# Kernel tuning notes

Measured on AMD Instinct MI355X. Metric: run time of the kernel, lower is better.

## Reference

```python
import jax, jax.numpy as jnp
import numpy as np

EPS = 1e-5


def _gcn_conv(h, W, b, src, dst, norm, N):
    # h: (B, N, F_in) -> linear transform then normalized neighbor aggregation
    h = h @ W                                  # (B, N, H)
    msg = h[:, src, :] * norm[None, :, None]   # gather + edge norm, (B, E, H)
    agg = jax.vmap(lambda m: jax.ops.segment_sum(m, dst, num_segments=N))(msg)
    return agg + b


def _batchnorm(h, gamma, beta):
    # BatchNorm1d over flattened (B*N, H), training-mode batch statistics
    B, N, H = h.shape
    f = h.reshape(-1, H)
    mean = f.mean(axis=0)
    var = f.var(axis=0)
    f = (f - mean) * jax.lax.rsqrt(var + EPS) * gamma + beta
    return f.reshape(B, N, H)


def setup_inputs() -> dict:
    key = jax.random.key(0)
    ks = jax.random.split(key, 6)
    B, N, E, IN, H, OUT = 2, 20000, 640000, 128, 128, 10
    x = jax.random.normal(ks[0], (B, N, IN), dtype=jnp.float32)
    edge_index = jax.random.randint(ks[1], (2, E), 0, N, dtype=jnp.int64)
    W1 = jax.random.normal(ks[2], (IN, H), dtype=jnp.float32) / np.sqrt(IN)
    W2 = jax.random.normal(ks[3], (H, H), dtype=jnp.float32) / np.sqrt(H)
    Wc = jax.random.normal(ks[4], (H, OUT), dtype=jnp.float32) / np.sqrt(H)
    return {
        "x": x,
        "W1": W1, "b1": jnp.zeros((H,), jnp.float32),
        "W2": W2, "b2": jnp.zeros((H,), jnp.float32),
        "g1": jnp.ones((H,), jnp.float32), "bt1": jnp.zeros((H,), jnp.float32),
        "g2": jnp.ones((H,), jnp.float32), "bt2": jnp.zeros((H,), jnp.float32),
        "Wc": Wc, "bc": jnp.zeros((OUT,), jnp.float32),
        "edge_index": edge_index,
    }


def reference(x, W1, b1, W2, b2, g1, bt1, g2, bt2, Wc, bc, edge_index):
    N = x.shape[1]
    loops = jnp.arange(N, dtype=edge_index.dtype)
    src = jnp.concatenate([edge_index[0], loops])  # add self-loops (GCNConv default)
    dst = jnp.concatenate([edge_index[1], loops])
    deg = jax.ops.segment_sum(jnp.ones(src.shape[0], x.dtype), dst, num_segments=N)
    dinv = jnp.where(deg > 0, jax.lax.rsqrt(deg), 0.0)
    norm = dinv[src] * dinv[dst]                   # symmetric GCN normalization

    h = jax.nn.relu(_gcn_conv(x, W1, b1, src, dst, norm, N))
    h = _batchnorm(h, g1, bt1)
    # dropout is identity in eval mode
    h = jax.nn.relu(_gcn_conv(h, W2, b2, src, dst, norm, N))
    h = _batchnorm(h, g2, bt2)
    return h @ Wc + bc                              # (B, N, out_dim)
```

## Files before the change

kernel.cpp:

```cpp
#include <hip/hip_runtime.h>
#include <hip/hip_bf16.h>


constexpr int Nn   = 20000;
constexpr int Ee   = 640000;
constexpr int OUTd = 10;
constexpr int Mm   = 2 * Nn;
constexpr int ELLW = 96;
constexpr int NSLOT = 64;
constexpr int NP   = 8;
constexpr int PSZ  = Nn / NP;
constexpr int NSEG = (Ee + 2047) / 2048;
constexpr int SCB  = NSEG * NP;
constexpr int GMB  = Mm / 64;
#define EPSV 1e-5f
constexpr float INV_M = 1.0f / (float)Mm;

using frag16 = __attribute__((ext_vector_type(8))) short;
using f32x4  = __attribute__((ext_vector_type(4))) float;

__device__ inline short bf(float f) {
    union { __hip_bfloat16 h; short s; } u;
    u.h = __float2bfloat16(f);
    return u.s;
}
__device__ inline float lo16(unsigned u) { union { unsigned v; float f; } x; x.v = u << 16;        return x.f; }
__device__ inline float hi16(unsigned u) { union { unsigned v; float f; } x; x.v = u & 0xffff0000u; return x.f; }
__device__ inline unsigned pack2(float f0, float f1) {
    return (unsigned)(unsigned short)bf(f0) | ((unsigned)(unsigned short)bf(f1) << 16);
}
__device__ inline float wdeg(int c) { return rsqrtf((float)c + 1.0f); }

__global__ __launch_bounds__(256) void fg1_k(const int* __restrict__ src, const int* __restrict__ dst,
                                             int* __restrict__ cnt, int* __restrict__ ell,
                                             const float* __restrict__ A,
                                             const float* __restrict__ W,
                                             unsigned short* __restrict__ Hout) {
    __shared__ short Wl[128 * 136];
    int t = threadIdx.x;

    if (blockIdx.x >= GMB) {
        int s   = blockIdx.x - GMB;
        int p   = blockIdx.x & 7;
        int seg = s >> 3;
        int lo  = p * PSZ, hi = lo + PSZ;
        int base = seg * 2048 + t;
        #pragma unroll
        for (int it = 0; it < 8; ++it) {
            int e = base + it * 256;
            if (e < Ee) {
                int d = dst[e];
                if (d >= lo && d < hi) {
                    int pos = atomicAdd(&cnt[d], 1);
                    if (pos < ELLW) ell[(size_t)d * ELLW + pos] = src[e];
                }
            }
        }
        return;
    }

    int bid = blockIdx.x;

    for (int it = 0; it < 8; ++it) {
        int lin = it * 256 + t;
        int kp  = lin & 63;
        int n4  = (lin >> 6) * 4;
        float4 w0 = *(const float4*)(W + (size_t)(2 * kp) * 128 + n4);
        float4 w1 = *(const float4*)(W + (size_t)(2 * kp + 1) * 128 + n4);
        *(unsigned*)&Wl[(n4 + 0) * 136 + 2 * kp] = pack2(w0.x, w1.x);
        *(unsigned*)&Wl[(n4 + 1) * 136 + 2 * kp] = pack2(w0.y, w1.y);
        *(unsigned*)&Wl[(n4 + 2) * 136 + 2 * kp] = pack2(w0.z, w1.z);
        *(unsigned*)&Wl[(n4 + 3) * 136 + 2 * kp] = pack2(w0.w, w1.w);
    }
    __syncthreads();

    int wv = t >> 6, l = t & 63;
    int row_q = l >> 4, lane16 = l & 15;
    int row0 = bid * 64 + wv * 16;

    frag16 a[4];
    const float* Arow = A + (size_t)(row0 + lane16) * 128;
    #pragma unroll
    for (int q = 0; q < 4; ++q) {
        int k0 = q * 32 + row_q * 8;
        float4 v0 = *(const float4*)(Arow + k0);
        float4 v1 = *(const float4*)(Arow + k0 + 4);
        frag16 fa = { bf(v0.x), bf(v0.y), bf(v0.z), bf(v0.w),
                      bf(v1.x), bf(v1.y), bf(v1.z), bf(v1.w) };
        a[q] = fa;
    }

    f32x4 acc[8];
    #pragma unroll
    for (int c = 0; c < 8; ++c) acc[c] = (f32x4){0.f, 0.f, 0.f, 0.f};

    #pragma unroll
    for (int c = 0; c < 8; ++c) {
        int n = c * 16 + lane16;
        #pragma unroll
        for (int q = 0; q < 4; ++q) {
            int k0 = q * 32 + row_q * 8;
            frag16 b = *(const frag16*)&Wl[n * 136 + k0];
            acc[c] = __builtin_amdgcn_mfma_f32_16x16x32_bf16(a[q], b, acc[c], 0, 0, 0);
        }
    }

    #pragma unroll
    for (int r = 0; r < 4; ++r) {
        int rg = row0 + row_q * 4 + r;
        int b  = rg >= Nn;
        int n  = rg - b * Nn;
        unsigned short* dstp = Hout + (size_t)n * 256 + b * 128;
        #pragma unroll
        for (int c = 0; c < 8; ++c)
            dstp[c * 16 + lane16] = (unsigned short)bf(acc[c][r]);
    }
}

__global__ __launch_bounds__(256) void gemm2_k(const unsigned short* __restrict__ Abf,
                                               const float* __restrict__ W,
                                               const float* __restrict__ g,
                                               const float* __restrict__ bt,
                                               const float* __restrict__ S,
                                               const int* __restrict__ cnt,
                                               unsigned short* __restrict__ Hout) {
    __shared__ short Wl[128 * 136];
    __shared__ float al[128], cl[128], dpart[2][128];
    int t = threadIdx.x;

    if (t < 128) {
        float s = 0.f, ss = 0.f;
        #pragma unroll 8
        for (int k = 0; k < NSLOT; ++k) {
            s  += S[k * 256 + t];
            ss += S[k * 256 + 128 + t];
        }
        float m   = s * INV_M;
        float var = ss * INV_M - m * m;
        float a   = g[t] * rsqrtf(var + EPSV);
        float c   = bt[t] - m * a;
        al[t] = a; cl[t] = c;
    }
    __syncthreads();

    for (int it = 0; it < 8; ++it) {
        int lin = it * 256 + t;
        int kp  = lin & 63;
        int n4  = (lin >> 6) * 4;
        float a0 = al[2 * kp], a1 = al[2 * kp + 1];
        float4 w0 = *(const float4*)(W + (size_t)(2 * kp) * 128 + n4);
        float4 w1 = *(const float4*)(W + (size_t)(2 * kp + 1) * 128 + n4);
        w0.x *= a0; w0.y *= a0; w0.z *= a0; w0.w *= a0;
        w1.x *= a1; w1.y *= a1; w1.z *= a1; w1.w *= a1;
        *(unsigned*)&Wl[(n4 + 0) * 136 + 2 * kp] = pack2(w0.x, w1.x);
        *(unsigned*)&Wl[(n4 + 1) * 136 + 2 * kp] = pack2(w0.y, w1.y);
        *(unsigned*)&Wl[(n4 + 2) * 136 + 2 * kp] = pack2(w0.z, w1.z);
        *(unsigned*)&Wl[(n4 + 3) * 136 + 2 * kp] = pack2(w0.w, w1.w);
    }

    {
        int col = t & 127, hh = t >> 7;
        const float* Wc0 = W + (size_t)(hh * 64) * 128 + col;
        float dp = 0.f;
        #pragma unroll 8
        for (int k = 0; k < 64; ++k) dp += cl[hh * 64 + k] * Wc0[(size_t)k * 128];
        dpart[hh][col] = dp;
    }
    __syncthreads();

    int wv = t >> 6, l = t & 63;
    int row_q = l >> 4, lane16 = l & 15;
    int row0 = blockIdx.x * 64 + wv * 16;

    int rgA = row0 + lane16;
    int bA  = rgA >= Nn;
    int nA  = rgA - bA * Nn;
    const unsigned short* Arow = Abf + (size_t)nA * 256 + bA * 128;
    frag16 a[4];
    #pragma unroll
    for (int q = 0; q < 4; ++q) {
        int k0 = q * 32 + row_q * 8;
        a[q] = *(const frag16*)(Arow + k0);
    }

    f32x4 acc[8];
    #pragma unroll
    for (int c = 0; c < 8; ++c) {
        int n = c * 16 + lane16;
        float d = dpart[0][n] + dpart[1][n];
        acc[c] = (f32x4){d, d, d, d};
    }

    #pragma unroll
    for (int c = 0; c < 8; ++c) {
        int n = c * 16 + lane16;
        #pragma unroll
        for (int q = 0; q < 4; ++q) {
            int k0 = q * 32 + row_q * 8;
            frag16 b = *(const frag16*)&Wl[n * 136 + k0];
            acc[c] = __builtin_amdgcn_mfma_f32_16x16x32_bf16(a[q], b, acc[c], 0, 0, 0);
        }
    }

    #pragma unroll
    for (int r = 0; r < 4; ++r) {
        int rg = row0 + row_q * 4 + r;
        int b  = rg >= Nn;
        int n  = rg - b * Nn;
        float dv = wdeg(cnt[n]);
        unsigned short* dst = Hout + (size_t)n * 256 + b * 128;
        #pragma unroll
        for (int c = 0; c < 8; ++c)
            dst[c * 16 + lane16] = (unsigned short)bf(acc[c][r] * dv);
    }
}

__device__ inline void accw(const uint4& v, float w,
                            float& a0, float& a1, float& a2, float& a3,
                            float& a4, float& a5, float& a6, float& a7) {
    a0 = fmaf(w, lo16(v.x), a0); a1 = fmaf(w, hi16(v.x), a1);
    a2 = fmaf(w, lo16(v.y), a2); a3 = fmaf(w, hi16(v.y), a3);
    a4 = fmaf(w, lo16(v.z), a4); a5 = fmaf(w, hi16(v.z), a5);
    a6 = fmaf(w, lo16(v.w), a6); a7 = fmaf(w, hi16(v.w), a7);
}
__device__ inline void acc8(const uint4& v,
                            float& a0, float& a1, float& a2, float& a3,
                            float& a4, float& a5, float& a6, float& a7) {
    a0 += lo16(v.x); a1 += hi16(v.x);
    a2 += lo16(v.y); a3 += hi16(v.y);
    a4 += lo16(v.z); a5 += hi16(v.z);
    a6 += lo16(v.w); a7 += hi16(v.w);
}

__device__ inline void stats_epilogue(int t, int wv, int l, int g, unsigned bslot,
                                      float o0, float o1, float o2, float o3,
                                      float o4, float o5, float o6, float o7,
                                      float* __restrict__ S) {
    float q0 = o0 * o0, q1 = o1 * o1, q2 = o2 * o2, q3 = o3 * o3;
    float q4 = o4 * o4, q5 = o5 * o5, q6 = o6 * o6, q7 = o7 * o7;
    float s0 = o0 + __shfl_xor(o0, 16), s1 = o1 + __shfl_xor(o1, 16);
    float s2 = o2 + __shfl_xor(o2, 16), s3 = o3 + __shfl_xor(o3, 16);
    float s4 = o4 + __shfl_xor(o4, 16), s5 = o5 + __shfl_xor(o5, 16);
    float s6 = o6 + __shfl_xor(o6, 16), s7 = o7 + __shfl_xor(o7, 16);
    float t0 = q0 + __shfl_xor(q0, 16), t1 = q1 + __shfl_xor(q1, 16);
    float t2 = q2 + __shfl_xor(q2, 16), t3 = q3 + __shfl_xor(q3, 16);
    float t4 = q4 + __shfl_xor(q4, 16), t5 = q5 + __shfl_xor(q5, 16);
    float t6 = q6 + __shfl_xor(q6, 16), t7 = q7 + __shfl_xor(q7, 16);

    __shared__ float sh[4][16][17];
    if (l < 16) {
        float* p = sh[wv][l];
        p[0] = s0; p[1] = s1; p[2] = s2; p[3] = s3;
        p[4] = s4; p[5] = s5; p[6] = s6; p[7] = s7;
        p[8]  = t0; p[9]  = t1; p[10] = t2; p[11] = t3;
        p[12] = t4; p[13] = t5; p[14] = t6; p[15] = t7;
    }
    __syncthreads();
    int col  = t & 127, stat = t >> 7;
    int gi   = col >> 3, slot = (col & 7) + stat * 8;
    float v = sh[0][gi][slot] + sh[1][gi][slot] + sh[2][gi][slot] + sh[3][gi][slot];
    atomicAdd(&S[bslot * 256 + stat * 128 + col], v);
}

__global__ __launch_bounds__(256) void agg1_k(const unsigned short* __restrict__ h,
                                              const int* __restrict__ ell,
                                              const int* __restrict__ cnt,
                                              const float* __restrict__ bias,
                                              unsigned short* __restrict__ act,
                                              float* __restrict__ S) {
    int t  = threadIdx.x;
    int wv = t >> 6;
    int l  = t & 63;
    int n  = __builtin_amdgcn_readfirstlane(blockIdx.x * 4 + wv);
    int half = l >> 5;
    int g    = l & 31;

    const uint4* h4 = (const uint4*)h;

    float a0 = 0.f, a1 = 0.f, a2 = 0.f, a3 = 0.f, a4 = 0.f, a5 = 0.f, a6 = 0.f, a7 = 0.f;

    int degc = cnt[n];
    float dn = wdeg(degc);
    int deg = degc > ELLW ? ELLW : degc;
    const int* row = ell + (size_t)n * ELLW;

    uint4 u = h4[(size_t)n * 32 + g];

    int j = 0;
    for (; j + 15 < deg; j += 16) {
        int i0 = row[j +  0 + half], i1 = row[j +  2 + half];
        int i2 = row[j +  4 + half], i3 = row[j +  6 + half];
        int i4 = row[j +  8 + half], i5 = row[j + 10 + half];
        int i6 = row[j + 12 + half], i7 = row[j + 14 + half];
        int c0 = cnt[i0], c1 = cnt[i1], c2 = cnt[i2], c3 = cnt[i3];
        int c4 = cnt[i4], c5 = cnt[i5], c6 = cnt[i6], c7 = cnt[i7];
        uint4 v0 = h4[(size_t)i0 * 32 + g];
        uint4 v1 = h4[(size_t)i1 * 32 + g];
        uint4 v2 = h4[(size_t)i2 * 32 + g];
        uint4 v3 = h4[(size_t)i3 * 32 + g];
        uint4 v4 = h4[(size_t)i4 * 32 + g];
        uint4 v5 = h4[(size_t)i5 * 32 + g];
        uint4 v6 = h4[(size_t)i6 * 32 + g];
        uint4 v7 = h4[(size_t)i7 * 32 + g];
        accw(v0, wdeg(c0), a0, a1, a2, a3, a4, a5, a6, a7);
        accw(v1, wdeg(c1), a0, a1, a2, a3, a4, a5, a6, a7);
        accw(v2, wdeg(c2), a0, a1, a2, a3, a4, a5, a6, a7);
        accw(v3, wdeg(c3), a0, a1, a2, a3, a4, a5, a6, a7);
        accw(v4, wdeg(c4), a0, a1, a2, a3, a4, a5, a6, a7);
        accw(v5, wdeg(c5), a0, a1, a2, a3, a4, a5, a6, a7);
        accw(v6, wdeg(c6), a0, a1, a2, a3, a4, a5, a6, a7);
        accw(v7, wdeg(c7), a0, a1, a2, a3, a4, a5, a6, a7);
    }
    for (; j + 3 < deg; j += 4) {
        int i0 = row[j + half];
        int i1 = row[j + 2 + half];
        int c0 = cnt[i0], c1 = cnt[i1];
        uint4 v0 = h4[(size_t)i0 * 32 + g];
        uint4 v1 = h4[(size_t)i1 * 32 + g];
        accw(v0, wdeg(c0), a0, a1, a2, a3, a4, a5, a6, a7);
        accw(v1, wdeg(c1), a0, a1, a2, a3, a4, a5, a6, a7);
    }
    for (; j + 1 < deg; j += 2) {
        int i0 = row[j + half];
        int c0 = cnt[i0];
        uint4 v0 = h4[(size_t)i0 * 32 + g];
        accw(v0, wdeg(c0), a0, a1, a2, a3, a4, a5, a6, a7);
    }
    if (j < deg && half == 0) {
        int i0 = row[j];
        int c0 = cnt[i0];
        uint4 v0 = h4[(size_t)i0 * 32 + g];
        accw(v0, wdeg(c0), a0, a1, a2, a3, a4, a5, a6, a7);
    }

    a0 += __shfl_xor(a0, 32); a1 += __shfl_xor(a1, 32);
    a2 += __shfl_xor(a2, 32); a3 += __shfl_xor(a3, 32);
    a4 += __shfl_xor(a4, 32); a5 += __shfl_xor(a5, 32);
    a6 += __shfl_xor(a6, 32); a7 += __shfl_xor(a7, 32);

    int cb   = (g & 15) * 8;
    float4 b0 = *(const float4*)(bias + cb);
    float4 b1 = *(const float4*)(bias + cb + 4);
    float i0v = fmaf(dn, lo16(u.x), a0), i1v = fmaf(dn, hi16(u.x), a1);
    float i2v = fmaf(dn, lo16(u.y), a2), i3v = fmaf(dn, hi16(u.y), a3);
    float i4v = fmaf(dn, lo16(u.z), a4), i5v = fmaf(dn, hi16(u.z), a5);
    float i6v = fmaf(dn, lo16(u.w), a6), i7v = fmaf(dn, hi16(u.w), a7);
    float o0 = fmaxf(fmaf(dn, i0v, b0.x), 0.f);
    float o1 = fmaxf(fmaf(dn, i1v, b0.y), 0.f);
    float o2 = fmaxf(fmaf(dn, i2v, b0.z), 0.f);
    float o3 = fmaxf(fmaf(dn, i3v, b0.w), 0.f);
    float o4 = fmaxf(fmaf(dn, i4v, b1.x), 0.f);
    float o5 = fmaxf(fmaf(dn, i5v, b1.y), 0.f);
    float o6 = fmaxf(fmaf(dn, i6v, b1.z), 0.f);
    float o7 = fmaxf(fmaf(dn, i7v, b1.w), 0.f);

    if (l < 32) {
        uint4 st;
        st.x = pack2(o0, o1); st.y = pack2(o2, o3);
        st.z = pack2(o4, o5); st.w = pack2(o6, o7);
        *(uint4*)(act + (size_t)n * 256 + (size_t)g * 8) = st;
    }

    stats_epilogue(t, wv, l, g, blockIdx.x & (NSLOT - 1),
                   o0, o1, o2, o3, o4, o5, o6, o7, S);
}

__global__ __launch_bounds__(256) void agg2_k(const unsigned short* __restrict__ h,
                                              const int* __restrict__ ell,
                                              const int* __restrict__ cnt,
                                              const float* __restrict__ bias,
                                              unsigned short* __restrict__ act,
                                              float* __restrict__ S) {
    int t  = threadIdx.x;
    int wv = t >> 6;
    int l  = t & 63;
    int n  = __builtin_amdgcn_readfirstlane(blockIdx.x * 4 + wv);
    int half = l >> 5;
    int g    = l & 31;

    const uint4* h4 = (const uint4*)h;

    float a0 = 0.f, a1 = 0.f, a2 = 0.f, a3 = 0.f, a4 = 0.f, a5 = 0.f, a6 = 0.f, a7 = 0.f;

    int degc = cnt[n];
    float dn = wdeg(degc);
    int deg = degc > ELLW ? ELLW : degc;
    const int* row = ell + (size_t)n * ELLW;

    uint4 u = h4[(size_t)n * 32 + g];

    int j = 0;
    for (; j + 15 < deg; j += 16) {
        int i0 = row[j +  0 + half], i1 = row[j +  2 + half];
        int i2 = row[j +  4 + half], i3 = row[j +  6 + half];
        int i4 = row[j +  8 + half], i5 = row[j + 10 + half];
        int i6 = row[j + 12 + half], i7 = row[j + 14 + half];
        uint4 v0 = h4[(size_t)i0 * 32 + g];
        uint4 v1 = h4[(size_t)i1 * 32 + g];
        uint4 v2 = h4[(size_t)i2 * 32 + g];
        uint4 v3 = h4[(size_t)i3 * 32 + g];
        uint4 v4 = h4[(size_t)i4 * 32 + g];
        uint4 v5 = h4[(size_t)i5 * 32 + g];
        uint4 v6 = h4[(size_t)i6 * 32 + g];
        uint4 v7 = h4[(size_t)i7 * 32 + g];
        acc8(v0, a0, a1, a2, a3, a4, a5, a6, a7);
        acc8(v1, a0, a1, a2, a3, a4, a5, a6, a7);
        acc8(v2, a0, a1, a2, a3, a4, a5, a6, a7);
        acc8(v3, a0, a1, a2, a3, a4, a5, a6, a7);
        acc8(v4, a0, a1, a2, a3, a4, a5, a6, a7);
        acc8(v5, a0, a1, a2, a3, a4, a5, a6, a7);
        acc8(v6, a0, a1, a2, a3, a4, a5, a6, a7);
        acc8(v7, a0, a1, a2, a3, a4, a5, a6, a7);
    }
    for (; j + 3 < deg; j += 4) {
        int i0 = row[j + half];
        int i1 = row[j + 2 + half];
        uint4 v0 = h4[(size_t)i0 * 32 + g];
        uint4 v1 = h4[(size_t)i1 * 32 + g];
        acc8(v0, a0, a1, a2, a3, a4, a5, a6, a7);
        acc8(v1, a0, a1, a2, a3, a4, a5, a6, a7);
    }
    for (; j + 1 < deg; j += 2) {
        int i0 = row[j + half];
        uint4 v0 = h4[(size_t)i0 * 32 + g];
        acc8(v0, a0, a1, a2, a3, a4, a5, a6, a7);
    }
    if (j < deg && half == 0) {
        int i0 = row[j];
        uint4 v0 = h4[(size_t)i0 * 32 + g];
        acc8(v0, a0, a1, a2, a3, a4, a5, a6, a7);
    }

    a0 += __shfl_xor(a0, 32); a1 += __shfl_xor(a1, 32);
    a2 += __shfl_xor(a2, 32); a3 += __shfl_xor(a3, 32);
    a4 += __shfl_xor(a4, 32); a5 += __shfl_xor(a5, 32);
    a6 += __shfl_xor(a6, 32); a7 += __shfl_xor(a7, 32);

    int cb   = (g & 15) * 8;
    float4 b0 = *(const float4*)(bias + cb);
    float4 b1 = *(const float4*)(bias + cb + 4);
    float o0 = fmaxf(fmaf(dn, a0 + lo16(u.x), b0.x), 0.f);
    float o1 = fmaxf(fmaf(dn, a1 + hi16(u.x), b0.y), 0.f);
    float o2 = fmaxf(fmaf(dn, a2 + lo16(u.y), b0.z), 0.f);
    float o3 = fmaxf(fmaf(dn, a3 + hi16(u.y), b0.w), 0.f);
    float o4 = fmaxf(fmaf(dn, a4 + lo16(u.z), b1.x), 0.f);
    float o5 = fmaxf(fmaf(dn, a5 + hi16(u.z), b1.y), 0.f);
    float o6 = fmaxf(fmaf(dn, a6 + lo16(u.w), b1.z), 0.f);
    float o7 = fmaxf(fmaf(dn, a7 + hi16(u.w), b1.w), 0.f);

    if (l < 32) {
        uint4 st;
        st.x = pack2(o0, o1); st.y = pack2(o2, o3);
        st.z = pack2(o4, o5); st.w = pack2(o6, o7);
        *(uint4*)(act + (size_t)n * 256 + (size_t)g * 8) = st;
    }

    stats_epilogue(t, wv, l, g, blockIdx.x & (NSLOT - 1),
                   o0, o1, o2, o3, o4, o5, o6, o7, S);
}

__global__ __launch_bounds__(256) void gemmout_k(const unsigned short* __restrict__ act,
                                                 const float* __restrict__ Wc,
                                                 const float* __restrict__ bc,
                                                 const float* __restrict__ g,
                                                 const float* __restrict__ bt,
                                                 const float* __restrict__ S,
                                                 float* __restrict__ out) {
    __shared__ float Wl[128 * OUTd];
    __shared__ float bl[OUTd];
    __shared__ float al[128], cl[128];
    int t = threadIdx.x;
    for (int i = t; i < 128 * OUTd; i += 256) Wl[i] = Wc[i];
    if (t < OUTd) bl[t] = bc[t];
    if (t < 128) {
        float s = 0.f, ss = 0.f;
        #pragma unroll 8
        for (int k = 0; k < NSLOT; ++k) {
            s  += S[k * 256 + t];
            ss += S[k * 256 + 128 + t];
        }
        float m   = s * INV_M;
        float var = ss * INV_M - m * m;
        float a   = g[t] * rsqrtf(var + EPSV);
        al[t] = a;
        cl[t] = bt[t] - m * a;
    }
    __syncthreads();

    int r = blockIdx.x * 256 + t;
    if (r >= Mm) return;
    int b = r >= Nn;
    int n = r - b * Nn;

    float acc[OUTd];
    #pragma unroll
    for (int jj = 0; jj < OUTd; jj++) acc[jj] = 0.f;

    const uint4* a4 = (const uint4*)(act + (size_t)n * 256 + b * 128);
    #pragma unroll 4
    for (int k4 = 0; k4 < 16; k4++) {
        uint4 u = a4[k4];
        int k = k4 * 8;
        float e0 = lo16(u.x) * al[k+0] + cl[k+0];
        float e1 = hi16(u.x) * al[k+1] + cl[k+1];
        float e2 = lo16(u.y) * al[k+2] + cl[k+2];
        float e3 = hi16(u.y) * al[k+3] + cl[k+3];
        float e4 = lo16(u.z) * al[k+4] + cl[k+4];
        float e5 = hi16(u.z) * al[k+5] + cl[k+5];
        float e6 = lo16(u.w) * al[k+6] + cl[k+6];
        float e7 = hi16(u.w) * al[k+7] + cl[k+7];
        #pragma unroll
        for (int jj = 0; jj < OUTd; jj++) {
            acc[jj] += e0 * Wl[(k+0) * OUTd + jj];
            acc[jj] += e1 * Wl[(k+1) * OUTd + jj];
            acc[jj] += e2 * Wl[(k+2) * OUTd + jj];
            acc[jj] += e3 * Wl[(k+3) * OUTd + jj];
            acc[jj] += e4 * Wl[(k+4) * OUTd + jj];
            acc[jj] += e5 * Wl[(k+5) * OUTd + jj];
            acc[jj] += e6 * Wl[(k+6) * OUTd + jj];
            acc[jj] += e7 * Wl[(k+7) * OUTd + jj];
        }
    }
    #pragma unroll
    for (int jj = 0; jj < OUTd; jj++) out[(size_t)r * OUTd + jj] = acc[jj] + bl[jj];
}

extern "C" void kernel_launch(void* const* d_in, const int* in_sizes, int n_in,
                              void* d_out, int out_size, void* d_ws, size_t ws_size,
                              hipStream_t stream) {
    (void)in_sizes; (void)n_in; (void)out_size; (void)ws_size;

    const float* x   = (const float*)d_in[0];
    const float* W1  = (const float*)d_in[1];
    const float* b1  = (const float*)d_in[2];
    const float* W2  = (const float*)d_in[3];
    const float* b2  = (const float*)d_in[4];
    const float* g1  = (const float*)d_in[5];
    const float* bt1 = (const float*)d_in[6];
    const float* g2  = (const float*)d_in[7];
    const float* bt2 = (const float*)d_in[8];
    const float* Wc  = (const float*)d_in[9];
    const float* bc  = (const float*)d_in[10];
    const int*   ei  = (const int*)d_in[11];
    const int* srcp = ei;
    const int* dstp = ei + Ee;

    char* ws = (char*)d_ws;
    size_t off = 0;
    auto alloc = [&](size_t bytes) -> void* {
        void* p = ws + off;
        off += (bytes + 511) & ~(size_t)511;
        return p;
    };
    unsigned short* h   = (unsigned short*)alloc((size_t)Mm * 128 * 2);
    unsigned short* act = (unsigned short*)alloc((size_t)Mm * 128 * 2);
    int*   cnt  = (int*)alloc(Nn * 4 + 2 * NSLOT * 256 * 4);
    float* S1   = (float*)(cnt + Nn);
    float* S2   = S1 + NSLOT * 256;
    int*   ell  = (int*)alloc((size_t)Nn * ELLW * 4);

    float* out = (float*)d_out;

    hipMemsetAsync(cnt, 0, Nn * 4 + 2 * NSLOT * 256 * 4, stream);
    fg1_k<<<GMB + SCB, 256, 0, stream>>>(srcp, dstp, cnt, ell, x, W1, h);

    agg1_k<<<Nn / 4, 256, 0, stream>>>(h, ell, cnt, b1, act, S1);

    gemm2_k<<<Mm / 64, 256, 0, stream>>>(act, W2, g1, bt1, S1, cnt, h);
    agg2_k<<<Nn / 4, 256, 0, stream>>>(h, ell, cnt, b2, act, S2);

    gemmout_k<<<(Mm + 255) / 256, 256, 0, stream>>>(act, Wc, bc, g2, bt2, S2, out);
}
```

Measured before the change: 241.1 us.

## Two-pass edge bucketing by destination partition before ELL scatter

Replaces the 8-way redundant edge scan in the fused GEMM/scatter kernel with a single pass that buckets (src,dst) pairs into 8 destination partitions using LDS counters and one global cursor atomic per partition. A new kernel then scatters each partition's pairs into the ELL structure with per-node atomics. This cuts the repeated reads of the edge list and keeps each scatter block's atomics within one destination range. In exchange it adds an extra launch and an intermediate pairs buffer, and it silently drops edges if a partition exceeds PCAP. The bucketing pass also reads edges without a bounds check, which is only safe because the edge count is an exact multiple of 1024.

```diff
diff --git a/kernel.cpp b/kernel.cpp
--- a/kernel.cpp
+++ b/kernel.cpp
@@ -10,9 +10,10 @@
 constexpr int NSLOT = 64;
 constexpr int NP   = 8;
 constexpr int PSZ  = Nn / NP;
-constexpr int NSEG = (Ee + 2047) / 2048;
-constexpr int SCB  = NSEG * NP;
+constexpr int PCAP = 98304;
 constexpr int GMB  = Mm / 64;
+constexpr int BKB  = (Ee + 1023) / 1024;
+constexpr int PBB  = 96;
 #define EPSV 1e-5f
 constexpr float INV_M = 1.0f / (float)Mm;
 
@@ -32,29 +33,38 @@
 __device__ inline float wdeg(int c) { return rsqrtf((float)c + 1.0f); }
 
 __global__ __launch_bounds__(256) void fg1_k(const int* __restrict__ src, const int* __restrict__ dst,
-                                             int* __restrict__ cnt, int* __restrict__ ell,
+                                             int* __restrict__ cursor, uint2* __restrict__ pairs,
                                              const float* __restrict__ A,
                                              const float* __restrict__ W,
                                              unsigned short* __restrict__ Hout) {
     __shared__ short Wl[128 * 136];
+    __shared__ int pcnt[NP];
+    __shared__ int pbase[NP];
     int t = threadIdx.x;
 
     if (blockIdx.x >= GMB) {
-        int s   = blockIdx.x - GMB;
-        int p   = blockIdx.x & 7;
-        int seg = s >> 3;
-        int lo  = p * PSZ, hi = lo + PSZ;
-        int base = seg * 2048 + t;
+        int s  = blockIdx.x - GMB;
+        int e0 = s * 1024;
+        if (t < NP) pcnt[t] = 0;
+        __syncthreads();
+        int es[4], ed[4], pp[4], pos[4];
         #pragma unroll
-        for (int it = 0; it < 8; ++it) {
-            int e = base + it * 256;
-            if (e < Ee) {
-                int d = dst[e];
-                if (d >= lo && d < hi) {
-                    int pos = atomicAdd(&cnt[d], 1);
-                    if (pos < ELLW) ell[(size_t)d * ELLW + pos] = src[e];
-                }
-            }
+        for (int it = 0; it < 4; ++it) {
+            int e = e0 + it * 256 + t;
+            int d = dst[e];
+            es[it] = src[e];
+            ed[it] = d;
+            pp[it] = (int)((unsigned)d / (unsigned)PSZ);
+            pos[it] = atomicAdd(&pcnt[pp[it]], 1);
+        }
+        __syncthreads();
+        if (t < NP) pbase[t] = atomicAdd(&cursor[t], pcnt[t]);
+        __syncthreads();
+        #pragma unroll
+        for (int it = 0; it < 4; ++it) {
+            int idx = pbase[pp[it]] + pos[it];
+            if (idx < PCAP)
+                pairs[(size_t)pp[it] * PCAP + idx] = make_uint2((unsigned)es[it], (unsigned)ed[it]);
         }
         return;
     }
@@ -114,6 +124,21 @@
         #pragma unroll
         for (int c = 0; c < 8; ++c)
             dstp[c * 16 + lane16] = (unsigned short)bf(acc[c][r]);
+    }
+}
+
+__global__ __launch_bounds__(256) void scat2_k(const uint2* __restrict__ pairs,
+                                               const int* __restrict__ cursor,
+                                               int* __restrict__ cnt, int* __restrict__ ell) {
+    int p     = blockIdx.x & (NP - 1);
+    int chunk = blockIdx.x >> 3;
+    int m = cursor[p]; if (m > PCAP) m = PCAP;
+    const uint2* bk = pairs + (size_t)p * PCAP;
+    for (int i = chunk * 256 + threadIdx.x; i < m; i += PBB * 256) {
+        uint2 pr = bk[i];
+        int d = (int)pr.y;
+        int pos = atomicAdd(&cnt[d], 1);
+        if (pos < ELLW) ell[(size_t)d * ELLW + pos] = (int)pr.x;
     }
 }
 
@@ -554,15 +579,19 @@
     };
     unsigned short* h   = (unsigned short*)alloc((size_t)Mm * 128 * 2);
     unsigned short* act = (unsigned short*)alloc((size_t)Mm * 128 * 2);
-    int*   cnt  = (int*)alloc(Nn * 4 + 2 * NSLOT * 256 * 4);
+    int*   cnt  = (int*)alloc(Nn * 4 + 2 * NSLOT * 256 * 4 + NP * 4);
     float* S1   = (float*)(cnt + Nn);
     float* S2   = S1 + NSLOT * 256;
+    int*   cursor = (int*)(S2 + NSLOT * 256);
     int*   ell  = (int*)alloc((size_t)Nn * ELLW * 4);
+    uint2* pairs = (uint2*)alloc((size_t)NP * PCAP * 8);
 
     float* out = (float*)d_out;
 
-    hipMemsetAsync(cnt, 0, Nn * 4 + 2 * NSLOT * 256 * 4, stream);
-    fg1_k<<<GMB + SCB, 256, 0, stream>>>(srcp, dstp, cnt, ell, x, W1, h);
+    hipMemsetAsync(cnt, 0, Nn * 4 + 2 * NSLOT * 256 * 4 + NP * 4, stream);
+    fg1_k<<<GMB + BKB, 256, 0, stream>>>(srcp, dstp, cursor, pairs, x, W1, h);
+
+    scat2_k<<<NP * PBB, 256, 0, stream>>>(pairs, cursor, cnt, ell);
 
     agg1_k<<<Nn / 4, 256, 0, stream>>>(h, ell, cnt, b1, act, S1);
 
```

Measured after the change: 243.5 us. No clear change (+1.0%).
